# Kernel tuning notes

Measured on AMD Instinct MI355X. Metric: run time of the kernel, lower is better.

Reference implementation:

```python
import jax, jax.numpy as jnp
import numpy as np

MAX_SEQ = 20          # text-token prefix length (config.max_seq_length)
NUM_HEADS = 12        # == num_spatial_relations
HEAD_DIM = 64         # 768 / 12
QUADRANTS = (1, 2, 4, 7, 8, 9)
NEG = -10000.0

BS, N_FEAT, D = 128, 182, 768   # N_FEAT = 20 text + 150 ocr/obj + 12 decode steps
R_OCR_OBJ = 150


def setup_inputs() -> dict:
    key = jax.random.key(0)
    ks = jax.random.split(key, 8)
    hidden_states = jax.random.normal(ks[0], (BS, N_FEAT, D), dtype=jnp.float32)
    attention_mask = jnp.where(
        jax.random.uniform(ks[1], (BS, 1, 1, N_FEAT)) < 0.9, 0.0, NEG
    ).astype(jnp.float32)
    # binary spatial relation adjacency (bs, R, R, 12)
    spatial_adj_matrix = jax.random.randint(
        ks[2], (BS, R_OCR_OBJ, R_OCR_OBJ, NUM_HEADS), 0, 2
    ).astype(jnp.float32)
    scale = 0.02
    Wq = jax.random.normal(ks[3], (D, D), dtype=jnp.float32) * scale
    Wk = jax.random.normal(ks[4], (D, D), dtype=jnp.float32) * scale
    Wv = jax.random.normal(ks[5], (D, D), dtype=jnp.float32) * scale
    bq = jnp.zeros((D,), jnp.float32)
    bk = jnp.zeros((D,), jnp.float32)
    bv = jnp.zeros((D,), jnp.float32)
    return {
        "hidden_states": hidden_states,
        "attention_mask": attention_mask,
        "spatial_adj_matrix": spatial_adj_matrix,
        "Wq": Wq, "bq": bq, "Wk": Wk, "bk": bk, "Wv": Wv, "bv": bv,
    }


def _spatial_additive_mask(spatial_adj_matrix, num_features, dtype):
    """Builds (bs, heads, N, N) additive mask in {0, -10000}, faithful to the
    sequential ones-fill / adjacency-copy / quadrant-zero / (1-m)*-10000 / permute."""
    bs, R = spatial_adj_matrix.shape[0], spatial_adj_matrix.shape[1]
    S = MAX_SEQ
    m = jnp.ones((bs, num_features, num_features, NUM_HEADS), dtype)
    m = m.at[:, S:S + R, S:S + R, :].set(spatial_adj_matrix.astype(dtype))
    for quad in QUADRANTS:  # num_spatial_relations == num_heads, so all head channels
        if quad == 1:
            m = m.at[:, :S, :S, :].set(0.0)
        elif quad == 2:
            m = m.at[:, :S, S:S + R, :].set(0.0)
        elif quad == 4:
            m = m.at[:, S:S + R, :S, :].set(0.0)
        elif quad == 7:
            m = m.at[:, S + R:, :S, :].set(0.0)
        elif quad == 8:
            m = m.at[:, S + R:, S:S + R, :].set(0.0)
        elif quad == 9:
            m = m.at[:, S + R:, S + R:, :].set(0.0)
    return jnp.transpose((1.0 - m) * NEG, (0, 3, 1, 2))  # (bs, H, N, N)


def _heads(x, bs, n):
    return jnp.transpose(x.reshape(bs, n, NUM_HEADS, HEAD_DIM), (0, 2, 1, 3))


def reference(hidden_states, attention_mask, spatial_adj_matrix,
              Wq, bq, Wk, bk, Wv, bv):
    bs, n, _ = hidden_states.shape
    spatial = _spatial_additive_mask(spatial_adj_matrix, n, hidden_states.dtype)
    # combined additive mask in {0, -10000}; attention_mask broadcasts (bs,1,1,N)
    combined = jnp.minimum(attention_mask, spatial)
    # 1.0 where a query row has at least one attendable key, else 0.0
    entity_probs_mask = (jnp.max(combined, axis=-1, keepdims=True) + 10000.0) / 10000.0

    q = _heads(hidden_states @ Wq.T + bq, bs, n)  # (bs, H, N, d)
    k = _heads(hidden_states @ Wk.T + bk, bs, n)
    v = _heads(hidden_states @ Wv.T + bv, bs, n)

    scores = jnp.einsum('bhqd,bhkd->bhqk', q, k) / 8.0 + combined  # sqrt(64)=8
    probs = jax.nn.softmax(scores, axis=-1) * entity_probs_mask
    ctx = jnp.einsum('bhqk,bhkd->bhqd', probs, v)
    ctx = jnp.transpose(ctx, (0, 2, 1, 3)).reshape(bs, n, NUM_HEADS * HEAD_DIM)
    return ctx
```

## Files before the change

### kernel.cpp

```cpp
#include <hip/hip_runtime.h>
#include <hip/hip_bf16.h>

#define NBS   128
#define NF    182
#define NP    192
#define DMODEL 768
#define NH    12
#define HDIM  64
#define SEQT  20
#define ROCR  150

typedef __attribute__((ext_vector_type(4))) float  f32x4;
typedef __attribute__((ext_vector_type(8))) short  s16x8;
using bf16 = __hip_bfloat16;

#define SB()    __builtin_amdgcn_sched_barrier(0)
#define BAR()   __builtin_amdgcn_s_barrier()

__device__ __forceinline__ void gload_lds16(const void* g, void* l) {
    auto gp = (const __attribute__((address_space(1))) unsigned int*)((unsigned long long)g);
    auto lp = (__attribute__((address_space(3))) unsigned int*)(unsigned int)((unsigned long long)l);
    __builtin_amdgcn_global_load_lds(gp, lp, 16, 0, 0);
}

__global__ __launch_bounds__(256) void convert_bf16(
    const float* __restrict__ hs,
    const float* __restrict__ Wq, const float* __restrict__ Wk, const float* __restrict__ Wv,
    bf16* __restrict__ hsb, bf16* __restrict__ Wb2)
{
    const size_t HT = (size_t)NBS * NF * DMODEL / 8;
    const size_t WT = 3ull * DMODEL * DMODEL / 8;
    size_t i = (size_t)blockIdx.x * 256 + threadIdx.x;
    if (i >= HT + WT) return;
    const float* src; bf16* dst;
    if (i < HT) {
        size_t e = i * 8; src = hs + e; dst = hsb + e;
    } else {
        size_t e = (i - HT) * 8;
        int R = (int)(e / DMODEL), c = (int)(e % DMODEL);
        int h = R / 192, t2 = (R % 192) / 64, r0 = R % 64;
        src = (t2 == 0 ? Wq : t2 == 1 ? Wk : Wv) + (size_t)(h * 64 + r0) * DMODEL + c;
        dst = Wb2 + e;
    }
    float4 a = *reinterpret_cast<const float4*>(src);
    float4 b = *reinterpret_cast<const float4*>(src + 4);
    union { s16x8 v; bf16 h8[8]; } u;
    u.h8[0] = __float2bfloat16(a.x); u.h8[1] = __float2bfloat16(a.y);
    u.h8[2] = __float2bfloat16(a.z); u.h8[3] = __float2bfloat16(a.w);
    u.h8[4] = __float2bfloat16(b.x); u.h8[5] = __float2bfloat16(b.y);
    u.h8[6] = __float2bfloat16(b.z); u.h8[7] = __float2bfloat16(b.w);
    *reinterpret_cast<s16x8*>(dst) = u.v;
}

__global__ __launch_bounds__(256) void pack_adj(const float* __restrict__ adj,
                                                unsigned long long* __restrict__ bits)
{
    __shared__ float tile[ROCR * NH];
    const int b = blockIdx.y, r = blockIdx.x;
    const int tid = threadIdx.x, lane = tid & 63, w = tid >> 6;
    const float* src = adj + ((size_t)b * ROCR + r) * (ROCR * NH);
    for (int i = tid; i < ROCR * NH; i += 256) tile[i] = src[i];
    __syncthreads();
    for (int c = w; c < NH * 3; c += 4) {
        int hh = c / 3, wd = c - hh * 3;
        int k = wd * 64 + lane;
        int j = k - SEQT;
        bool v = false;
        if (j >= 0 && j < ROCR) v = (tile[j * NH + hh] > 0.5f);
        unsigned long long m = __ballot(v);
        if (lane == 0) bits[(((size_t)b * NH + hh) * ROCR + r) * 3 + wd] = m;
    }
}

#define KO2   0
#define VTO2  24576
#define QO2   49152
#define PO2   49152
#define LWO2  73728
#define AWO2  78336

__global__ __launch_bounds__(256, 2) void fused_qkv_attn(
    const bf16* __restrict__ hsb, const bf16* __restrict__ Wb2,
    const float* __restrict__ bq, const float* __restrict__ bk, const float* __restrict__ bv,
    const float* __restrict__ amask,
    const unsigned long long* __restrict__ bits,
    float* __restrict__ out)
{
    __shared__ char L[78368];
    const int tid  = threadIdx.x;
    const int lane = tid & 63;
    const int wid  = tid >> 6;
    const int wr = wid >> 1, wc = wid & 1;
    const int lm = lane & 15, lg = lane >> 4;

    const int flat = blockIdx.x;
    const int wgid = (flat & 7) * 192 + (flat >> 3);
    const int b = wgid / NH, h = wgid - b * NH;

    float* obase = out + (size_t)b * NF * DMODEL + h * HDIM;

    if (wid == 0) {
        #pragma unroll
        for (int w = 0; w < 3; ++w) {
            int k = w * 64 + lane;
            bool v = (k < NF) && (amask[b * NF + k] == 0.0f);
            unsigned long long m = __ballot(v);
            if (lane == 0) ((unsigned long long*)(L + AWO2))[w] = m;
        }
    }
    for (int i = tid; i < 12 * 64; i += 256)
        obase[(size_t)(170 + (i >> 6)) * DMODEL + (i & 63)] = 0.f;
    __syncthreads();
    if (tid < NP) {
        int r = tid;
        unsigned long long s0 = 0, s1 = 0, s2 = 0;
        const unsigned long long DEC = 0xFFFull << 42;
        if (r < SEQT) {
            s2 = DEC;
        } else if (r < SEQT + ROCR) {
            const unsigned long long* bp = bits + (((size_t)b * NH + h) * ROCR + (r - SEQT)) * 3;
            s0 = bp[0]; s1 = bp[1]; s2 = bp[2] | DEC;
        }
        unsigned long long* aw = (unsigned long long*)(L + AWO2);
        unsigned long long* Lw = (unsigned long long*)(L + LWO2);
        Lw[r * 3 + 0] = s0 & aw[0];
        Lw[r * 3 + 1] = s1 & aw[1];
        Lw[r * 3 + 2] = s2 & aw[2];
    }

    const char* gA = (const char*)(hsb + (size_t)b * NF * DMODEL);
    const char* gW = (const char*)(Wb2 + (size_t)h * 192 * DMODEL);

    f32x4 acc[6][6];
    #pragma unroll
    for (int i = 0; i < 6; ++i)
        #pragma unroll
        for (int j = 0; j < 6; ++j) acc[i][j] = (f32x4){0.f, 0.f, 0.f, 0.f};

    const int srow4 = tid >> 2, sch4 = tid & 3;

    auto ST = [&](int kt, int bsel) {
        char* dA = L + bsel * 24576;
        char* dW = dA + 12288;
        #pragma unroll
        for (int it = 0; it < 3; ++it) {
            int row = it * 64 + srow4;
            int lc = sch4 ^ ((row >> 1) & 3);
            size_t go = (size_t)row * 1536 + (size_t)kt * 64 + lc * 16;
            int o = row * 64 + sch4 * 16;
            gload_lds16(gA + go, dA + o);
            gload_lds16(gW + go, dW + o);
        }
    };
    auto CP = [&](int bsel) {
        const char* Ab = L + bsel * 24576;
        const char* Wp = Ab + 12288;
        s16x8 af[6], bf6[6];
        #pragma unroll
        for (int mi = 0; mi < 6; ++mi) {
            int r = 96 * wr + 16 * mi + lm;
            af[mi] = *reinterpret_cast<const s16x8*>(Ab + r * 64 + ((lg ^ ((r >> 1) & 3)) << 4));
        }
        #pragma unroll
        for (int ni = 0; ni < 6; ++ni) {
            int r = 96 * wc + 16 * ni + lm;
            bf6[ni] = *reinterpret_cast<const s16x8*>(Wp + r * 64 + ((lg ^ ((r >> 1) & 3)) << 4));
        }
        __builtin_amdgcn_s_setprio(1);
        #pragma unroll
        for (int mi = 0; mi < 6; ++mi)
            #pragma unroll
            for (int ni = 0; ni < 6; ++ni)
                acc[mi][ni] = __builtin_amdgcn_mfma_f32_16x16x32_bf16(af[mi], bf6[ni], acc[mi][ni], 0, 0, 0);
        __builtin_amdgcn_s_setprio(0);
    };

    ST(0, 0);
    ST(1, 1);
    for (int t = 0; t < 24; ++t) {
        if (t < 23) { asm volatile("s_waitcnt vmcnt(6)" ::: "memory"); }
        else        { asm volatile("s_waitcnt vmcnt(0)" ::: "memory"); }
        SB(); BAR(); SB();
        CP(t & 1);
        SB(); BAR();
        if (t + 2 < 24) ST(t + 2, t & 1);
    }
    BAR();

    float bias6[6];
    #pragma unroll
    for (int ni = 0; ni < 6; ++ni) {
        int c = 96 * wc + 16 * ni + lm;
        int whichc = c >> 6, cc = c & 63;
        const float* bp = (whichc == 0) ? bq : (whichc == 1) ? bk : bv;
        bias6[ni] = bp[h * 64 + cc];
    }
    #pragma unroll
    for (int mi = 0; mi < 6; ++mi) {
        #pragma unroll
        for (int ni = 0; ni < 6; ++ni) {
            int c = 96 * wc + 16 * ni + lm;
            #pragma unroll
            for (int j = 0; j < 4; ++j) {
                int row = 96 * wr + 16 * mi + 4 * lg + j;
                bf16 hv = __float2bfloat16(acc[mi][ni][j] + bias6[ni]);
                unsigned short us = *reinterpret_cast<unsigned short*>(&hv);
                if (c < 64) {
                    *reinterpret_cast<unsigned short*>(L + QO2 + row * 128 + ((2 * c) ^ ((row & 7) << 4))) = us;
                } else if (c < 128) {
                    int cc = c - 64;
                    *reinterpret_cast<unsigned short*>(L + KO2 + row * 128 + ((2 * cc) ^ ((row & 7) << 4))) = us;
                } else if (row < NF) {
                    int d = c - 128;
                    *reinterpret_cast<unsigned short*>(L + VTO2 + d * 384 + ((2 * row) ^ ((d & 7) << 4))) = us;
                }
            }
        }
    }
    for (int i = tid; i < 64 * 10; i += 256) {
        int d = i / 10, k2 = NF + (i - d * 10);
        *reinterpret_cast<unsigned short*>(L + VTO2 + d * 384 + ((2 * k2) ^ ((d & 7) << 4))) = 0;
    }
    __syncthreads();

    s16x8 qf[3][2];
    #pragma unroll
    for (int bi = 0; bi < 3; ++bi) {
        int band = wid + 4 * bi;
        int qrow = ((band < 11) ? band : 0) * 16 + lm;
        const char* qb = L + QO2 + qrow * 128;
        int sq = (qrow & 7) << 4;
        qf[bi][0] = *reinterpret_cast<const s16x8*>(qb + ((lg * 16) ^ sq));
        qf[bi][1] = *reinterpret_cast<const s16x8*>(qb + ((64 + lg * 16) ^ sq));
    }
    __syncthreads();

    const unsigned long long* LwA = (const unsigned long long*)(L + LWO2);
    char* Pw = L + PO2 + wid * 6144;

    #pragma unroll
    for (int bi = 0; bi < 3; ++bi) {
        const int band = wid + 4 * bi;
        if (band >= 11) continue;
        const int q0 = band * 16;

        f32x4 sacc[12];
        #pragma unroll
        for (int t = 0; t < 12; ++t) sacc[t] = (f32x4){0.f, 0.f, 0.f, 0.f};
        #pragma unroll
        for (int t = 0; t < 12; ++t) {
            int key = t * 16 + lm;
            const char* kb = L + KO2 + key * 128;
            int sw = (key & 7) << 4;
            s16x8 kf0 = *reinterpret_cast<const s16x8*>(kb + ((lg * 16) ^ sw));
            s16x8 kf1 = *reinterpret_cast<const s16x8*>(kb + ((64 + lg * 16) ^ sw));
            sacc[t] = __builtin_amdgcn_mfma_f32_16x16x32_bf16(qf[bi][0], kf0, sacc[t], 0, 0, 0);
            sacc[t] = __builtin_amdgcn_mfma_f32_16x16x32_bf16(qf[bi][1], kf1, sacc[t], 0, 0, 0);
        }

        float scl[4];
        #pragma unroll
        for (int j = 0; j < 4; ++j) {
            int row = q0 + lg * 4 + j;
            unsigned long long w0 = LwA[row * 3 + 0], w1 = LwA[row * 3 + 1], w2 = LwA[row * 3 + 2];
            float mx = -3.0e38f;
            #pragma unroll
            for (int t = 0; t < 12; ++t) {
                unsigned long long w = (t < 4) ? w0 : (t < 8) ? w1 : w2;
                int sh = ((t & 3) << 4) + lm;
                float s = sacc[t][j] * 0.125f;
                s = ((w >> sh) & 1ull) ? s : -3.0e38f;
                sacc[t][j] = s;
                mx = fmaxf(mx, s);
            }
            mx = fmaxf(mx, __shfl_xor(mx, 1));
            mx = fmaxf(mx, __shfl_xor(mx, 2));
            mx = fmaxf(mx, __shfl_xor(mx, 4));
            mx = fmaxf(mx, __shfl_xor(mx, 8));
            float sum = 0.f;
            #pragma unroll
            for (int t = 0; t < 12; ++t) {
                float e = (sacc[t][j] > -1.0e37f) ? __expf(sacc[t][j] - mx) : 0.f;
                sacc[t][j] = e;
                sum += e;
            }
            sum += __shfl_xor(sum, 1);
            sum += __shfl_xor(sum, 2);
            sum += __shfl_xor(sum, 4);
            sum += __shfl_xor(sum, 8);
            scl[j] = (mx > -1.0e37f) ? 1.0f / sum : 0.f;
        }

        #pragma unroll
        for (int j = 0; j < 4; ++j) {
            int prow = lg * 4 + j;
            int sw = (prow & 7) << 4;
            char* prb = Pw + prow * 384;
            #pragma unroll
            for (int t = 0; t < 12; ++t) {
                bf16 pv = __float2bfloat16(sacc[t][j] * scl[j]);
                *reinterpret_cast<unsigned short*>(prb + (((t * 16 + lm) * 2) ^ sw)) =
                    *reinterpret_cast<unsigned short*>(&pv);
            }
        }
        asm volatile("s_waitcnt lgkmcnt(0)" ::: "memory");
        __builtin_amdgcn_sched_barrier(0);

        f32x4 oacc[4];
        #pragma unroll
        for (int t = 0; t < 4; ++t) oacc[t] = (f32x4){0.f, 0.f, 0.f, 0.f};
        int psw = (lm & 7) << 4;
        #pragma unroll
        for (int ks = 0; ks < 6; ++ks) {
            s16x8 pf = *reinterpret_cast<const s16x8*>(Pw + lm * 384 + ((ks * 64 + lg * 16) ^ psw));
            #pragma unroll
            for (int t = 0; t < 4; ++t) {
                int d = t * 16 + lm;
                s16x8 vf = *reinterpret_cast<const s16x8*>(L + VTO2 + d * 384 + ((ks * 64 + lg * 16) ^ ((d & 7) << 4)));
                oacc[t] = __builtin_amdgcn_mfma_f32_16x16x32_bf16(pf, vf, oacc[t], 0, 0, 0);
            }
        }
        #pragma unroll
        for (int j = 0; j < 4; ++j) {
            int row = q0 + lg * 4 + j;
            if (row < 170) {
                #pragma unroll
                for (int t = 0; t < 4; ++t)
                    obase[(size_t)row * DMODEL + t * 16 + lm] = oacc[t][j];
            }
        }
    }
}

extern "C" void kernel_launch(void* const* d_in, const int* in_sizes, int n_in,
                              void* d_out, int out_size, void* d_ws, size_t ws_size,
                              hipStream_t stream)
{
    const float* hs    = (const float*)d_in[0];
    const float* amask = (const float*)d_in[1];
    const float* adj   = (const float*)d_in[2];
    const float* Wq    = (const float*)d_in[3];
    const float* bq    = (const float*)d_in[4];
    const float* Wk    = (const float*)d_in[5];
    const float* bk    = (const float*)d_in[6];
    const float* Wv    = (const float*)d_in[7];
    const float* bv    = (const float*)d_in[8];
    float* out = (float*)d_out;

    char* ws = (char*)d_ws;
    bf16* Wb2 = (bf16*)ws;
    unsigned long long* bits = (unsigned long long*)(ws + 3538944);
    bf16* hsb = (bf16*)(ws + 3538944 + 5529600);

    const int cvt_blocks = (int)(((size_t)NBS * NF * DMODEL / 8 + 3ull * DMODEL * DMODEL / 8 + 255) / 256);
    convert_bf16<<<cvt_blocks, 256, 0, stream>>>(hs, Wq, Wk, Wv, hsb, Wb2);
    pack_adj<<<dim3(ROCR, NBS), 256, 0, stream>>>(adj, bits);
    fused_qkv_attn<<<dim3(NBS * NH), 256, 0, stream>>>(hsb, Wb2, bq, bk, bv, amask, bits, out);
}
```

Measured before the change: 220.9 us.

## Replace direct global-to-LDS double buffer with register-staged single buffer, K=64 tiles

```diff
diff --git a/kernel.cpp b/kernel.cpp
--- a/kernel.cpp
+++ b/kernel.cpp
@@ -16,12 +16,7 @@
 
 #define SB()    __builtin_amdgcn_sched_barrier(0)
 #define BAR()   __builtin_amdgcn_s_barrier()
-
-__device__ __forceinline__ void gload_lds16(const void* g, void* l) {
-    auto gp = (const __attribute__((address_space(1))) unsigned int*)((unsigned long long)g);
-    auto lp = (__attribute__((address_space(3))) unsigned int*)(unsigned int)((unsigned long long)l);
-    __builtin_amdgcn_global_load_lds(gp, lp, 16, 0, 0);
-}
+#define LGKM0() asm volatile("s_waitcnt lgkmcnt(0)" ::: "memory")
 
 __global__ __launch_bounds__(256) void convert_bf16(
     const float* __restrict__ hs,
@@ -137,55 +132,77 @@
         #pragma unroll
         for (int j = 0; j < 6; ++j) acc[i][j] = (f32x4){0.f, 0.f, 0.f, 0.f};
 
-    const int srow4 = tid >> 2, sch4 = tid & 3;
-
-    auto ST = [&](int kt, int bsel) {
-        char* dA = L + bsel * 24576;
-        char* dW = dA + 12288;
-        #pragma unroll
-        for (int it = 0; it < 3; ++it) {
-            int row = it * 64 + srow4;
-            int lc = sch4 ^ ((row >> 1) & 3);
-            size_t go = (size_t)row * 1536 + (size_t)kt * 64 + lc * 16;
-            int o = row * 64 + sch4 * 16;
-            gload_lds16(gA + go, dA + o);
-            gload_lds16(gW + go, dW + o);
+    const int srow8 = tid >> 3, sch8 = tid & 7;
+
+    s16x8 ra0, ra1, ra2, ra3, ra4, ra5;
+    s16x8 rw0, rw1, rw2, rw3, rw4, rw5;
+
+    auto LDR = [&](int kt) {
+        #pragma unroll
+        for (int it = 0; it < 6; ++it) {
+            int row = it * 32 + srow8;
+            int lc = sch8 ^ (row & 7);
+            size_t go = (size_t)row * 1536 + (size_t)kt * 128 + lc * 16;
+            s16x8 va = *reinterpret_cast<const s16x8*>(gA + go);
+            s16x8 vw = *reinterpret_cast<const s16x8*>(gW + go);
+            switch (it) {
+                case 0: ra0 = va; rw0 = vw; break;
+                case 1: ra1 = va; rw1 = vw; break;
+                case 2: ra2 = va; rw2 = vw; break;
+                case 3: ra3 = va; rw3 = vw; break;
+                case 4: ra4 = va; rw4 = vw; break;
+                case 5: ra5 = va; rw5 = vw; break;
+            }
         }
     };
-    auto CP = [&](int bsel) {
-        const char* Ab = L + bsel * 24576;
-        const char* Wp = Ab + 12288;
-        s16x8 af[6], bf6[6];
-        #pragma unroll
-        for (int mi = 0; mi < 6; ++mi) {
-            int r = 96 * wr + 16 * mi + lm;
-            af[mi] = *reinterpret_cast<const s16x8*>(Ab + r * 64 + ((lg ^ ((r >> 1) & 3)) << 4));
-        }
-        #pragma unroll
-        for (int ni = 0; ni < 6; ++ni) {
-            int r = 96 * wc + 16 * ni + lm;
-            bf6[ni] = *reinterpret_cast<const s16x8*>(Wp + r * 64 + ((lg ^ ((r >> 1) & 3)) << 4));
-        }
-        __builtin_amdgcn_s_setprio(1);
-        #pragma unroll
-        for (int mi = 0; mi < 6; ++mi)
+    auto WRT = [&]() {
+        #pragma unroll
+        for (int it = 0; it < 6; ++it) {
+            int o = (it * 32 + srow8) * 128 + sch8 * 16;
+            s16x8 va = (it == 0) ? ra0 : (it == 1) ? ra1 : (it == 2) ? ra2
+                     : (it == 3) ? ra3 : (it == 4) ? ra4 : ra5;
+            s16x8 vw = (it == 0) ? rw0 : (it == 1) ? rw1 : (it == 2) ? rw2
+                     : (it == 3) ? rw3 : (it == 4) ? rw4 : rw5;
+            *reinterpret_cast<s16x8*>(L + o) = va;
+            *reinterpret_cast<s16x8*>(L + 24576 + o) = vw;
+        }
+    };
+    auto CP = [&]() {
+        const char* Ab = L;
+        const char* Wp = L + 24576;
+        #pragma unroll
+        for (int kk = 0; kk < 2; ++kk) {
+            int coff = ((kk * 4 + lg) ^ (lm & 7)) << 4;
+            s16x8 af[6], bf6[6];
+            #pragma unroll
+            for (int mi = 0; mi < 6; ++mi)
+                af[mi] = *reinterpret_cast<const s16x8*>(Ab + (96 * wr + 16 * mi + lm) * 128 + coff);
             #pragma unroll
             for (int ni = 0; ni < 6; ++ni)
-                acc[mi][ni] = __builtin_amdgcn_mfma_f32_16x16x32_bf16(af[mi], bf6[ni], acc[mi][ni], 0, 0, 0);
-        __builtin_amdgcn_s_setprio(0);
+                bf6[ni] = *reinterpret_cast<const s16x8*>(Wp + (96 * wc + 16 * ni + lm) * 128 + coff);
+            __builtin_amdgcn_s_setprio(1);
+            #pragma unroll
+            for (int mi = 0; mi < 6; ++mi)
+                #pragma unroll
+                for (int ni = 0; ni < 6; ++ni)
+                    acc[mi][ni] = __builtin_amdgcn_mfma_f32_16x16x32_bf16(af[mi], bf6[ni], acc[mi][ni], 0, 0, 0);
+            __builtin_amdgcn_s_setprio(0);
+        }
     };
 
-    ST(0, 0);
-    ST(1, 1);
-    for (int t = 0; t < 24; ++t) {
-        if (t < 23) { asm volatile("s_waitcnt vmcnt(6)" ::: "memory"); }
-        else        { asm volatile("s_waitcnt vmcnt(0)" ::: "memory"); }
-        SB(); BAR(); SB();
-        CP(t & 1);
+    LDR(0);
+    WRT();
+    LGKM0();
+    BAR();
+
+    for (int t = 0; t < 12; ++t) {
+        if (t < 11) LDR(t + 1);
+        SB();
+        CP();
         SB(); BAR();
-        if (t + 2 < 24) ST(t + 2, t & 1);
-    }
-    BAR();
+        if (t < 11) { WRT(); LGKM0(); }
+        SB(); BAR();
+    }
 
     float bias6[6];
     #pragma unroll
```

Measured after the change: 261.6 us. +18.4%, slower.

## Spill V-transpose to global scratch to cut LDS and raise occupancy to 3 blocks

Applied to the files above, without the earlier changes.

```diff
diff --git a/kernel.cpp b/kernel.cpp
--- a/kernel.cpp
+++ b/kernel.cpp
@@ -72,21 +72,21 @@
     }
 }
 
-#define KO2   0
-#define VTO2  24576
-#define QO2   49152
-#define PO2   49152
-#define LWO2  73728
-#define AWO2  78336
-
-__global__ __launch_bounds__(256, 2) void fused_qkv_attn(
+#define KO3   0
+#define QO3   24576
+#define PO3   24576
+#define LWO3  49152
+#define AWO3  53376
+
+__global__ __launch_bounds__(256, 3) void fused_qkv_attn(
     const bf16* __restrict__ hsb, const bf16* __restrict__ Wb2,
     const float* __restrict__ bq, const float* __restrict__ bk, const float* __restrict__ bv,
     const float* __restrict__ amask,
     const unsigned long long* __restrict__ bits,
+    bf16* __restrict__ vtg,
     float* __restrict__ out)
 {
-    __shared__ char L[78368];
+    __shared__ char L[53408];
     const int tid  = threadIdx.x;
     const int lane = tid & 63;
     const int wid  = tid >> 6;
@@ -98,6 +98,7 @@
     const int b = wgid / NH, h = wgid - b * NH;
 
     float* obase = out + (size_t)b * NF * DMODEL + h * HDIM;
+    bf16*  vtb   = vtg + (size_t)wgid * HDIM * NP;
 
     if (wid == 0) {
         #pragma unroll
@@ -105,13 +106,13 @@
             int k = w * 64 + lane;
             bool v = (k < NF) && (amask[b * NF + k] == 0.0f);
             unsigned long long m = __ballot(v);
-            if (lane == 0) ((unsigned long long*)(L + AWO2))[w] = m;
+            if (lane == 0) ((unsigned long long*)(L + AWO3))[w] = m;
         }
     }
     for (int i = tid; i < 12 * 64; i += 256)
         obase[(size_t)(170 + (i >> 6)) * DMODEL + (i & 63)] = 0.f;
     __syncthreads();
-    if (tid < NP) {
+    if (tid < 176) {
         int r = tid;
         unsigned long long s0 = 0, s1 = 0, s2 = 0;
         const unsigned long long DEC = 0xFFFull << 42;
@@ -121,8 +122,8 @@
             const unsigned long long* bp = bits + (((size_t)b * NH + h) * ROCR + (r - SEQT)) * 3;
             s0 = bp[0]; s1 = bp[1]; s2 = bp[2] | DEC;
         }
-        unsigned long long* aw = (unsigned long long*)(L + AWO2);
-        unsigned long long* Lw = (unsigned long long*)(L + LWO2);
+        unsigned long long* aw = (unsigned long long*)(L + AWO3);
+        unsigned long long* Lw = (unsigned long long*)(L + LWO3);
         Lw[r * 3 + 0] = s0 & aw[0];
         Lw[r * 3 + 1] = s1 & aw[1];
         Lw[r * 3 + 2] = s2 & aw[2];
@@ -200,26 +201,38 @@
         #pragma unroll
         for (int ni = 0; ni < 6; ++ni) {
             int c = 96 * wc + 16 * ni + lm;
-            #pragma unroll
-            for (int j = 0; j < 4; ++j) {
-                int row = 96 * wr + 16 * mi + 4 * lg + j;
-                bf16 hv = __float2bfloat16(acc[mi][ni][j] + bias6[ni]);
-                unsigned short us = *reinterpret_cast<unsigned short*>(&hv);
-                if (c < 64) {
-                    *reinterpret_cast<unsigned short*>(L + QO2 + row * 128 + ((2 * c) ^ ((row & 7) << 4))) = us;
-                } else if (c < 128) {
-                    int cc = c - 64;
-                    *reinterpret_cast<unsigned short*>(L + KO2 + row * 128 + ((2 * cc) ^ ((row & 7) << 4))) = us;
-                } else if (row < NF) {
-                    int d = c - 128;
-                    *reinterpret_cast<unsigned short*>(L + VTO2 + d * 384 + ((2 * row) ^ ((d & 7) << 4))) = us;
+            int row0 = 96 * wr + 16 * mi + 4 * lg;
+            if (c < 128) {
+                #pragma unroll
+                for (int j = 0; j < 4; ++j) {
+                    int row = row0 + j;
+                    bf16 hv = __float2bfloat16(acc[mi][ni][j] + bias6[ni]);
+                    unsigned short us = *reinterpret_cast<unsigned short*>(&hv);
+                    if (c < 64) {
+                        if (row < 176)
+                            *reinterpret_cast<unsigned short*>(L + QO3 + row * 128 + ((2 * c) ^ ((row & 7) << 4))) = us;
+                    } else {
+                        int cc = c - 64;
+                        *reinterpret_cast<unsigned short*>(L + KO3 + row * 128 + ((2 * cc) ^ ((row & 7) << 4))) = us;
+                    }
                 }
-            }
-        }
-    }
-    for (int i = tid; i < 64 * 10; i += 256) {
-        int d = i / 10, k2 = NF + (i - d * 10);
-        *reinterpret_cast<unsigned short*>(L + VTO2 + d * 384 + ((2 * k2) ^ ((d & 7) << 4))) = 0;
+            } else {
+                int d = c - 128;
+                float v0 = (row0 + 0 < NF) ? acc[mi][ni][0] + bias6[ni] : 0.f;
+                float v1 = (row0 + 1 < NF) ? acc[mi][ni][1] + bias6[ni] : 0.f;
+                float v2 = (row0 + 2 < NF) ? acc[mi][ni][2] + bias6[ni] : 0.f;
+                float v3 = (row0 + 3 < NF) ? acc[mi][ni][3] + bias6[ni] : 0.f;
+                bf16 b0 = __float2bfloat16(v0), b1 = __float2bfloat16(v1);
+                bf16 b2 = __float2bfloat16(v2), b3 = __float2bfloat16(v3);
+                unsigned int w01 = ((unsigned int)*reinterpret_cast<unsigned short*>(&b1) << 16)
+                                 |  (unsigned int)*reinterpret_cast<unsigned short*>(&b0);
+                unsigned int w23 = ((unsigned int)*reinterpret_cast<unsigned short*>(&b3) << 16)
+                                 |  (unsigned int)*reinterpret_cast<unsigned short*>(&b2);
+                unsigned int* dst = reinterpret_cast<unsigned int*>(vtb + (size_t)d * NP + row0);
+                dst[0] = w01;
+                dst[1] = w23;
+            }
+        }
     }
     __syncthreads();
 
@@ -228,15 +241,15 @@
     for (int bi = 0; bi < 3; ++bi) {
         int band = wid + 4 * bi;
         int qrow = ((band < 11) ? band : 0) * 16 + lm;
-        const char* qb = L + QO2 + qrow * 128;
+        const char* qb = L + QO3 + qrow * 128;
         int sq = (qrow & 7) << 4;
         qf[bi][0] = *reinterpret_cast<const s16x8*>(qb + ((lg * 16) ^ sq));
         qf[bi][1] = *reinterpret_cast<const s16x8*>(qb + ((64 + lg * 16) ^ sq));
     }
     __syncthreads();
 
-    const unsigned long long* LwA = (const unsigned long long*)(L + LWO2);
-    char* Pw = L + PO2 + wid * 6144;
+    const unsigned long long* LwA = (const unsigned long long*)(L + LWO3);
+    char* Pw = L + PO3 + wid * 6144;
 
     #pragma unroll
     for (int bi = 0; bi < 3; ++bi) {
@@ -250,7 +263,7 @@
         #pragma unroll
         for (int t = 0; t < 12; ++t) {
             int key = t * 16 + lm;
-            const char* kb = L + KO2 + key * 128;
+            const char* kb = L + KO3 + key * 128;
             int sw = (key & 7) << 4;
             s16x8 kf0 = *reinterpret_cast<const s16x8*>(kb + ((lg * 16) ^ sw));
             s16x8 kf1 = *reinterpret_cast<const s16x8*>(kb + ((64 + lg * 16) ^ sw));
@@ -316,7 +329,7 @@
             #pragma unroll
             for (int t = 0; t < 4; ++t) {
                 int d = t * 16 + lm;
-                s16x8 vf = *reinterpret_cast<const s16x8*>(L + VTO2 + d * 384 + ((ks * 64 + lg * 16) ^ ((d & 7) << 4)));
+                s16x8 vf = *reinterpret_cast<const s16x8*>(vtb + (size_t)d * NP + ks * 32 + lg * 8);
                 oacc[t] = __builtin_amdgcn_mfma_f32_16x16x32_bf16(pf, vf, oacc[t], 0, 0, 0);
             }
         }
@@ -351,9 +364,10 @@
     bf16* Wb2 = (bf16*)ws;
     unsigned long long* bits = (unsigned long long*)(ws + 3538944);
     bf16* hsb = (bf16*)(ws + 3538944 + 5529600);
+    bf16* vtg = (bf16*)(ws + 3538944 + 5529600 + 35782656);
 
     const int cvt_blocks = (int)(((size_t)NBS * NF * DMODEL / 8 + 3ull * DMODEL * DMODEL / 8 + 255) / 256);
     convert_bf16<<<cvt_blocks, 256, 0, stream>>>(hs, Wq, Wk, Wv, hsb, Wb2);
     pack_adj<<<dim3(ROCR, NBS), 256, 0, stream>>>(adj, bits);
-    fused_qkv_attn<<<dim3(NBS * NH), 256, 0, stream>>>(hsb, Wb2, bq, bk, bv, amask, bits, out);
-}
+    fused_qkv_attn<<<dim3(NBS * NH), 256, 0, stream>>>(hsb, Wb2, bq, bk, bv, amask, bits, vtg, out);
+}
```

Result: slower. 723.7 us (+227.5%).
